# Kernel optimization log

Hardware: AMD Instinct MI355X
Metric: run time of the kernel (lower is better)

Reference implementation:

```python
import jax, jax.numpy as jnp
import numpy as np

B, N, IN_DIM, OUT = 4, 4096, 3, 40
NPTS = [1024, 256, 64, 16]   # base_points // sampling_ratio
K, FIRST_K = 8, 16
EPS = 1e-5

def gelu(t):
    return jax.nn.gelu(t, approximate=False)  # torch nn.GELU default (erf)

def pdist2(a, b):
    # a: (b,d,m), b: (b,d,n) -> squared pairwise distances (b,m,n)
    aa = jnp.sum(a * a, axis=1)[:, :, None]
    bb = jnp.sum(b * b, axis=1)[:, None, :]
    return aa + bb - 2.0 * jnp.einsum('bdm,bdn->bmn', a, b)

def knn_idx(a, b, k):
    # indices of k nearest points of b for each point of a
    return jax.lax.top_k(-pdist2(a, b), k)[1]

def gather_nbr(x, ind):
    # x: (b,d,n), ind: (b,m,k) -> (b,d,m,k)
    b, d, n = x.shape
    m, k = ind.shape[1], ind.shape[2]
    idx = jnp.broadcast_to(ind.reshape(b, 1, m * k), (b, d, m * k))
    return jnp.take_along_axis(x, idx, axis=2).reshape(b, d, m, k)

def bn(x):
    # BatchNorm (training-mode batch stats, gamma=1, beta=0 as at init)
    ax = (0,) + tuple(range(2, x.ndim))
    mu = jnp.mean(x, axis=ax, keepdims=True)
    var = jnp.mean((x - mu) ** 2, axis=ax, keepdims=True)
    return (x - mu) / jnp.sqrt(var + EPS)

def route(x, nbr):
    # (b,d,n),(b,n,k) -> (b,2d,n,k) : cat([neighbor - center, center])
    sel = gather_nbr(x, nbr)
    xc = x[:, :, :, None]
    return jnp.concatenate([sel - xc, jnp.broadcast_to(xc, sel.shape)], axis=1)

def edge_conv(x, l1, l2, sc, k, nbr=None):
    if nbr is None:
        nbr = knn_idx(x, x, k)  # dynamic graph in feature space
    h = jnp.max(jnp.einsum('of,bfnk->bonk', l1, route(x, nbr)), axis=-1)
    h = gelu(bn(h))
    h = jnp.max(jnp.einsum('of,bfnk->bonk', l2, route(h, nbr)), axis=-1)
    short = x if sc is None else jnp.einsum('of,bfn->bon', sc, x)
    return gelu(bn(short + h))

def fps(xyz, m):
    # farthest point sampling; xyz: (b,3,n) -> indices (b,m); start index 0
    pts = jnp.transpose(xyz, (0, 2, 1))  # (b,n,3)
    b, n, _ = pts.shape
    def body(carry, _):
        dmin, last = carry
        lp = jnp.take_along_axis(pts, last[:, None, None], axis=1)  # (b,1,3)
        d = jnp.sum((pts - lp) ** 2, axis=-1)
        dmin = jnp.minimum(dmin, d)
        nxt = jnp.argmax(dmin, axis=-1).astype(jnp.int32)
        return (dmin, nxt), last
    init = (jnp.full((b, n), jnp.inf, pts.dtype), jnp.zeros((b,), jnp.int32))
    _, inds = jax.lax.scan(body, init, None, length=m)
    return jnp.transpose(inds)  # (b,m)

def _forward(x, xyz, mlp_w, mlp_b, c0_l1, c0_l2, l1s, l2s, scs,
             head_w1, head_w2, head_b2):
    b = x.shape[0]
    nbr0 = knn_idx(xyz, xyz, FIRST_K)
    h = gelu(bn(jnp.einsum('oi,bin->bon', mlp_w, x) + mlp_b[None, :, None]))
    h = edge_conv(h, c0_l1, c0_l2, None, FIRST_K, nbr=nbr0)
    cur = xyz
    for i in range(4):
        m = NPTS[i]
        sind = fps(cur, m)
        sxyz = jnp.take_along_axis(
            cur, jnp.broadcast_to(sind[:, None, :], (b, cur.shape[1], m)), axis=2)
        nbr = knn_idx(sxyz, cur, K)
        cur = jnp.mean(gather_nbr(cur, nbr), axis=-1)      # sampled xyz = nbr mean
        h = jnp.max(gather_nbr(h, nbr), axis=-1)           # sampled feat = nbr max
        h = edge_conv(h, l1s[i], l2s[i], scs[i], K)
    g = jnp.mean(h, axis=-1)                               # global average pool
    g = gelu(bn(g @ head_w1.T))
    return g @ head_w2.T + head_b2[None, :]


def setup_inputs() -> dict:
    key = jax.random.key(0)
    ks = jax.random.split(key, 20)
    def w(k, o, i):
        return (jax.random.normal(k, (o, i), jnp.float32) / np.sqrt(i)).astype(jnp.float32)
    return {
        'x': jax.random.normal(ks[0], (B, IN_DIM, N), jnp.float32),
        'xyz': jax.random.normal(ks[1], (B, 3, N), jnp.float32),
        'mlp_w': w(ks[2], 64, IN_DIM), 'mlp_b': jnp.zeros((64,), jnp.float32),
        'c0_l1': w(ks[3], 64, 128), 'c0_l2': w(ks[4], 64, 128),
        's0_l1': w(ks[5], 64, 128), 's0_l2': w(ks[6], 64, 128),
        's1_l1': w(ks[7], 128, 128), 's1_l2': w(ks[8], 128, 256), 's1_sc': w(ks[9], 128, 64),
        's2_l1': w(ks[10], 256, 256), 's2_l2': w(ks[11], 256, 512), 's2_sc': w(ks[12], 256, 128),
        's3_l1': w(ks[13], 512, 512), 's3_l2': w(ks[14], 512, 1024), 's3_sc': w(ks[15], 512, 256),
        'head_w1': w(ks[16], 256, 512), 'head_w2': w(ks[17], OUT, 256),
        'head_b2': jnp.zeros((OUT,), jnp.float32),
    }


def reference(x, xyz, mlp_w, mlp_b, c0_l1, c0_l2, s0_l1, s0_l2,
              s1_l1, s1_l2, s1_sc, s2_l1, s2_l2, s2_sc, s3_l1, s3_l2, s3_sc,
              head_w1, head_w2, head_b2):
    return _forward(x, xyz, mlp_w, mlp_b, c0_l1, c0_l2,
                    (s0_l1, s1_l1, s2_l1, s3_l1),
                    (s0_l2, s1_l2, s2_l2, s3_l2),
                    (None, s1_sc, s2_sc, s3_sc),
                    head_w1, head_w2, head_b2)
```

## Files before the change

### kernel.cpp

```cpp
#include <hip/hip_runtime.h>
#include <math.h>

#define NCHUNK 32
typedef unsigned long long ull;

__device__ __forceinline__ float gelu_f(float v){
  return 0.5f*v*(1.0f+erff(v*0.70710678118654752440f));
}

__device__ __forceinline__ unsigned flipf(float d){
  unsigned u = __float_as_uint(d);
  return (u & 0x80000000u) ? ~u : (u | 0x80000000u);
}

__device__ __forceinline__ ull umin64(ull a, ull b){ return a < b ? a : b; }
__device__ __forceinline__ ull umax64(ull a, ull b){ return a > b ? a : b; }

template<int CTRL>
__device__ __forceinline__ ull dpp64(ull k){
  int lo = __builtin_amdgcn_update_dpp(0, (int)(unsigned)k,       CTRL, 0xF, 0xF, true);
  int hi = __builtin_amdgcn_update_dpp(0, (int)(unsigned)(k>>32), CTRL, 0xF, 0xF, true);
  return ((ull)(unsigned)hi<<32) | (unsigned)lo;
}
__device__ __forceinline__ ull rl64(ull k, int l){
  unsigned lo = (unsigned)__builtin_amdgcn_readlane((int)(unsigned)k, l);
  unsigned hi = (unsigned)__builtin_amdgcn_readlane((int)(unsigned)(k>>32), l);
  return ((ull)hi<<32) | lo;
}
__device__ __forceinline__ ull fmax64(ull a, ull b){
  return (ull)__double_as_longlong(fmax(__longlong_as_double((long long)a),
                                        __longlong_as_double((long long)b)));
}
__device__ __forceinline__ ull wave_fmax(ull k){
  k = fmax64(k, dpp64<0xB1>(k));
  k = fmax64(k, dpp64<0x4E>(k));
  k = fmax64(k, dpp64<0x141>(k));
  k = fmax64(k, dpp64<0x140>(k));
  ull a=rl64(k,0), b=rl64(k,16), c=rl64(k,32), d=rl64(k,48);
  return fmax64(fmax64(a,b), fmax64(c,d));
}
template<int CTRL>
__device__ __forceinline__ ull kmin_dpp(ull k){
  ull o = dpp64<CTRL>(k);
  return o < k ? o : k;
}
__device__ __forceinline__ ull wave_kmin(ull k){
  k = kmin_dpp<0xB1>(k);
  k = kmin_dpp<0x4E>(k);
  k = kmin_dpp<0x141>(k);
  k = kmin_dpp<0x140>(k);
  ull a=rl64(k,0), b=rl64(k,16), c=rl64(k,32), d=rl64(k,48);
  ull ab = a < b ? a : b, cd = c < d ? c : d;
  return ab < cd ? ab : cd;
}


template<int K, int T>
__device__ __forceinline__ void knn_body(
    const float* __restrict__ cand, int n,
    const float* __restrict__ qsrc, const int* __restrict__ qidx, int m,
    int* __restrict__ nbr, float* __restrict__ outc,
    int b, int qblk, int qoff, char* smem)
{
  float4* tile = (float4*)smem;
  constexpr int NWV = T/64;
  int wv = threadIdx.x >> 6, lane = threadIdx.x & 63;
  int q = qblk*NWV + wv + qoff;
  const float* cb = cand + (size_t)b*3*n;
  int qi = qidx ? qidx[(size_t)b*m + q] : q;
  const float* qb = qsrc + (size_t)b*3*n;
  float qx = qb[qi], qy = qb[n+qi], qz = qb[2*n+qi];
  float aa = (qx*qx + qy*qy) + qz*qz;

  ull a[K];
  #pragma unroll
  for (int k=0;k<K;k++) a[k] = ~0ull;

  for (int base=0; base<n; base+=1024){
    int cnt = min(1024, n-base);
    for (int j=threadIdx.x; j<cnt; j+=T){
      float x=cb[base+j], y=cb[n+base+j], z=cb[2*n+base+j];
      tile[j] = make_float4(x,y,z,(x*x+y*y)+z*z);
    }
    __syncthreads();
    int steps = cnt >> 6;
    for (int i=0;i<steps;i++){
      int j = lane + (i<<6);
      float4 c = tile[j];
      float d = aa + c.w - 2.0f*((qx*c.x+qy*c.y)+qz*c.z);
      ull key = ((ull)flipf(d)<<32) | (unsigned)(base+j);
      if (key < a[K-1]){
        #pragma unroll
        for (int k=K-1;k>=1;k--)
          a[k] = umin64(umax64(a[k-1], key), a[k]);
        a[0] = umin64(a[0], key);
      }
    }
    __syncthreads();
  }

  ull head = a[0];
  int res[K];
  #pragma unroll
  for (int r=0; r<K; r++){
    ull mk = wave_kmin(head);
    res[r] = (int)(unsigned)mk;
    if (head == mk){
      #pragma unroll
      for (int i2=0;i2<K-1;i2++) a[i2]=a[i2+1];
      a[K-1] = ~0ull;
      head = a[0];
    }
  }
  if (lane == 0){
    int* o = nbr + ((size_t)b*m + q)*K;
    #pragma unroll
    for (int r=0;r<K;r++) o[r] = res[r];
  }
  if (outc != nullptr && lane < 3){
    const float* cd = cb + (size_t)lane*n;
    float s=0;
    #pragma unroll
    for (int k=0;k<K;k++) s += cd[res[k]];
    outc[((size_t)b*3 + lane)*m + q] = s * (1.0f/K);
  }
}

template<int NP, int T, int M>
__device__ __forceinline__ void fps_mw_seg(const float* __restrict__ cur, int n,
                                           int* __restrict__ sind, float* __restrict__ gdmin,
                                           int b, int M0, int M1, char* smem)
{
  constexpr int NW = T/64;
  int tid = threadIdx.x;
  int wv = tid>>6;
  const float* cb = cur + (size_t)b*3*n;
  float4* lp = (float4*)smem;
  ull* wred = (ull*)(smem + sizeof(float4)*NP*T);
  float* gd = gdmin + (size_t)b*n;
  float px[NP], py[NP], pz[NP], dmin[NP];
  unsigned nj[NP];
  #pragma unroll
  for (int s=0;s<NP;s++){
    int j = tid + s*T;
    px[s]=cb[j]; py[s]=cb[n+j]; pz[s]=cb[2*n+j];
    dmin[s] = (M0==0) ? 1e30f : gd[j];
    nj[s] = (unsigned)(~j);
    lp[j] = make_float4(px[s],py[s],pz[s],0.f);
  }
  __syncthreads();
  int ci = (M0==0) ? 0 : sind[(size_t)b*M + (M0-1)];
  float4 w0 = lp[ci];
  float X = w0.x, Y = w0.y, Z = w0.z;
  if (M0==0 && tid==0) sind[(size_t)b*M] = 0;
  __builtin_amdgcn_s_setprio(3);
  int p = 0;
  int s0 = (M0==0) ? 1 : M0;
  for (int step=s0; step<M1; step++){
    ull key[NP];
    #pragma unroll
    for (int s=0;s<NP;s++){
      float dx=px[s]-X, dy=py[s]-Y, dz=pz[s]-Z;
      float d = (dx*dx + dy*dy) + dz*dz;
      float nd = fminf(dmin[s], d);
      dmin[s] = nd;
      key[s] = ((ull)__float_as_uint(nd)<<32) | nj[s];
    }
    #pragma unroll
    for (int w=NP; w>1; w>>=1)
      #pragma unroll
      for (int i=0;i<NP;i++) if (i < (w>>1))
        key[i] = fmax64(key[i], key[i+(w>>1)]);
    ull wk = wave_fmax(key[0]);
    if ((tid&63)==0) wred[p*NW + wv] = wk;
    __syncthreads();
    const ulonglong2* wp2 = (const ulonglong2*)(wred + p*NW);
    ulonglong2 m0 = wp2[0], m1 = wp2[1], m2 = wp2[2], m3 = wp2[3];
    ull gk = fmax64(fmax64(fmax64(m0.x,m0.y), fmax64(m1.x,m1.y)),
                    fmax64(fmax64(m2.x,m2.y), fmax64(m3.x,m3.y)));
    int gi = (int)(~(unsigned)gk);
    if (tid==0) sind[(size_t)b*M + step] = gi;
    float4 wp = lp[gi];
    X=wp.x; Y=wp.y; Z=wp.z;
    p ^= 1;
  }
  __builtin_amdgcn_s_setprio(0);
  #pragma unroll
  for (int s=0;s<NP;s++) gd[tid + s*T] = dmin[s];
}

template<int NP, int M>
__device__ __forceinline__ void fps_sw_body(const float* __restrict__ cur, int n,
                                            int* __restrict__ sind, int b, char* smem)
{
  int lane = threadIdx.x;
  const float* cb = cur + (size_t)b*3*n;
  float4* lp = (float4*)smem;
  float px[NP], py[NP], pz[NP], dmin[NP];
  unsigned nj[NP];
  #pragma unroll
  for (int s=0;s<NP;s++){
    int j = lane + s*64;
    px[s]=cb[j]; py[s]=cb[n+j]; pz[s]=cb[2*n+j]; dmin[s]=1e30f;
    nj[s] = (unsigned)(~j);
    lp[j] = make_float4(px[s],py[s],pz[s],0.f);
  }
  float X = lp[0].x, Y = lp[0].y, Z = lp[0].z;
  if (lane==0) sind[(size_t)b*M] = 0;
  __builtin_amdgcn_s_setprio(3);
  for (int step=1; step<M; step++){
    ull key[NP];
    #pragma unroll
    for (int s=0;s<NP;s++){
      float dx=px[s]-X, dy=py[s]-Y, dz=pz[s]-Z;
      float d = (dx*dx + dy*dy) + dz*dz;
      float nd = fminf(dmin[s], d);
      dmin[s] = nd;
      key[s] = ((ull)__float_as_uint(nd)<<32) | nj[s];
    }
    #pragma unroll
    for (int w=NP; w>1; w>>=1)
      #pragma unroll
      for (int i=0;i<NP;i++) if (i < (w>>1))
        key[i] = fmax64(key[i], key[i+(w>>1)]);
    ull gk = wave_fmax(key[0]);
    int gi = (int)(~(unsigned)gk);
    if (lane==0) sind[(size_t)b*M + step] = gi;
    float4 wp = lp[gi];
    X=wp.x; Y=wp.y; Z=wp.z;
  }
  __builtin_amdgcn_s_setprio(0);
}

template<bool DUAL, bool BN>
__device__ __forceinline__ void gemm_body(
    const float* __restrict__ A, const float* __restrict__ B,
    float* __restrict__ out0, float* __restrict__ out1,
    int M, int N, int Kd, int lda, int ldb, int ldo, int boff,
    long sA, long sB, long sO, const float* __restrict__ part, float invR,
    int bxi, int byi, int bzi, char* smem)
{
  A += (size_t)bzi * sA; B += (size_t)bzi * sB;
  float* o0 = out0 + (size_t)bzi * sO;
  float* o1 = DUAL ? (out1 + (size_t)bzi * sO) : nullptr;
  int rowBase = byi*64, colBase = bxi*64;
  float (*As)[64]  = (float(*)[64])smem;
  float (*Bs0)[64] = (float(*)[64])(smem + 4096);
  float (*Bs1)[64] = (float(*)[64])(smem + 8192);
  float* mu_s = (float*)(smem + 12288);
  float* var_s = mu_s + 512;
  int tid = threadIdx.x;
  if (BN){
    for (int oo=tid; oo<Kd; oo+=blockDim.x){
      float s=0, q=0;
      #pragma unroll 4
      for (int c=0;c<NCHUNK;c++){
        s += part[(size_t)c*1024 + oo];
        q += part[(size_t)(NCHUNK+c)*1024 + oo];
      }
      float mu = s*invR;
      mu_s[oo] = mu;
      var_s[oo] = q*invR - mu*mu;
    }
    __syncthreads();
  }
  int ty = tid>>4, tx = tid&15;
  float acc0[4][4] = {}, acc1[4][4] = {};
  int lr = tid>>2, lk = (tid&3)*4;
  for (int k0=0; k0<Kd; k0+=16) {
    float4 va = make_float4(0,0,0,0);
    int r = rowBase + lr;
    if (r < M) va = *(const float4*)(A + (size_t)r*lda + k0 + lk);
    if (BN){
      int c = k0 + lk;
      va.x = gelu_f((va.x - mu_s[c+0]) / sqrtf(var_s[c+0] + 1e-5f));
      va.y = gelu_f((va.y - mu_s[c+1]) / sqrtf(var_s[c+1] + 1e-5f));
      va.z = gelu_f((va.z - mu_s[c+2]) / sqrtf(var_s[c+2] + 1e-5f));
      va.w = gelu_f((va.w - mu_s[c+3]) / sqrtf(var_s[c+3] + 1e-5f));
    }
    As[lk+0][lr]=va.x; As[lk+1][lr]=va.y; As[lk+2][lr]=va.z; As[lk+3][lr]=va.w;
    float4 vb = make_float4(0,0,0,0), vb2 = make_float4(0,0,0,0);
    int c2 = colBase + lr;
    if (c2 < N) {
      vb = *(const float4*)(B + (size_t)c2*ldb + k0 + lk);
      if (DUAL) vb2 = *(const float4*)(B + (size_t)c2*ldb + boff + k0 + lk);
    }
    Bs0[lk+0][lr]=vb.x; Bs0[lk+1][lr]=vb.y; Bs0[lk+2][lr]=vb.z; Bs0[lk+3][lr]=vb.w;
    if (DUAL) {
      Bs1[lk+0][lr]=vb2.x-vb.x; Bs1[lk+1][lr]=vb2.y-vb.y;
      Bs1[lk+2][lr]=vb2.z-vb.z; Bs1[lk+3][lr]=vb2.w-vb.w;
    }
    __syncthreads();
    #pragma unroll
    for (int kk=0;kk<16;kk++){
      float4 a  = *(const float4*)&As[kk][ty*4];
      float4 b0 = *(const float4*)&Bs0[kk][tx*4];
      float av[4]={a.x,a.y,a.z,a.w};
      float b0v[4]={b0.x,b0.y,b0.z,b0.w};
      #pragma unroll
      for (int i=0;i<4;i++)
        #pragma unroll
        for (int j=0;j<4;j++) acc0[i][j] = fmaf(av[i], b0v[j], acc0[i][j]);
      if (DUAL) {
        float4 b1 = *(const float4*)&Bs1[kk][tx*4];
        float b1v[4]={b1.x,b1.y,b1.z,b1.w};
        #pragma unroll
        for (int i=0;i<4;i++)
          #pragma unroll
          for (int j=0;j<4;j++) acc1[i][j] = fmaf(av[i], b1v[j], acc1[i][j]);
      }
    }
    __syncthreads();
  }
  #pragma unroll
  for (int i=0;i<4;i++){
    int r = rowBase + ty*4 + i;
    if (r < M) {
      #pragma unroll
      for (int j=0;j<4;j++){
        int c = colBase + tx*4 + j;
        if (c < N) {
          o0[(size_t)r*ldo + c] = acc0[i][j];
          if (DUAL) o1[(size_t)r*ldo + c] = acc1[i][j];
        }
      }
    }
  }
}

template<bool DUAL, bool BN>
__device__ __forceinline__ void gemm_body_g(
    const float* __restrict__ A, const float* __restrict__ B,
    float* __restrict__ out0, float* __restrict__ out1,
    int M, int N, int Kd, int lda, int ldb, int ldo, int boff,
    const float* __restrict__ part, float invR,
    int bxi, int byi, char* smem)
{
  int rowBase = byi*64, colBase = bxi*64;
  float (*As)[64]  = (float(*)[64])smem;
  float (*Bs0)[64] = (float(*)[64])(smem + 4096);
  float (*Bs1)[64] = (float(*)[64])(smem + 8192);
  float* mu_s = (float*)(smem + 12288);
  float* var_s = mu_s + 512;
  int tid = threadIdx.x;
  bool act = tid < 256;
  if (BN){
    for (int oo=tid; oo<Kd; oo+=blockDim.x){
      float s=0, q=0;
      #pragma unroll 4
      for (int c=0;c<NCHUNK;c++){
        s += part[(size_t)c*1024 + oo];
        q += part[(size_t)(NCHUNK+c)*1024 + oo];
      }
      float mu = s*invR;
      mu_s[oo] = mu;
      var_s[oo] = q*invR - mu*mu;
    }
    __syncthreads();
  }
  int ty = tid>>4, tx = tid&15;
  float acc0[4][4] = {}, acc1[4][4] = {};
  int lr = tid>>2, lk = (tid&3)*4;
  for (int k0=0; k0<Kd; k0+=16) {
    if (act){
      float4 va = make_float4(0,0,0,0);
      int r = rowBase + lr;
      if (r < M) va = *(const float4*)(A + (size_t)r*lda + k0 + lk);
      if (BN){
        int c = k0 + lk;
        va.x = gelu_f((va.x - mu_s[c+0]) / sqrtf(var_s[c+0] + 1e-5f));
        va.y = gelu_f((va.y - mu_s[c+1]) / sqrtf(var_s[c+1] + 1e-5f));
        va.z = gelu_f((va.z - mu_s[c+2]) / sqrtf(var_s[c+2] + 1e-5f));
        va.w = gelu_f((va.w - mu_s[c+3]) / sqrtf(var_s[c+3] + 1e-5f));
      }
      As[lk+0][lr]=va.x; As[lk+1][lr]=va.y; As[lk+2][lr]=va.z; As[lk+3][lr]=va.w;
      float4 vb = make_float4(0,0,0,0), vb2 = make_float4(0,0,0,0);
      int c2 = colBase + lr;
      if (c2 < N) {
        vb = *(const float4*)(B + (size_t)c2*ldb + k0 + lk);
        if (DUAL) vb2 = *(const float4*)(B + (size_t)c2*ldb + boff + k0 + lk);
      }
      Bs0[lk+0][lr]=vb.x; Bs0[lk+1][lr]=vb.y; Bs0[lk+2][lr]=vb.z; Bs0[lk+3][lr]=vb.w;
      if (DUAL) {
        Bs1[lk+0][lr]=vb2.x-vb.x; Bs1[lk+1][lr]=vb2.y-vb.y;
        Bs1[lk+2][lr]=vb2.z-vb.z; Bs1[lk+3][lr]=vb2.w-vb.w;
      }
    }
    __syncthreads();
    if (act){
      #pragma unroll
      for (int kk=0;kk<16;kk++){
        float4 a  = *(const float4*)&As[kk][ty*4];
        float4 b0 = *(const float4*)&Bs0[kk][tx*4];
        float av[4]={a.x,a.y,a.z,a.w};
        float b0v[4]={b0.x,b0.y,b0.z,b0.w};
        #pragma unroll
        for (int i=0;i<4;i++)
          #pragma unroll
          for (int j=0;j<4;j++) acc0[i][j] = fmaf(av[i], b0v[j], acc0[i][j]);
        if (DUAL) {
          float4 b1 = *(const float4*)&Bs1[kk][tx*4];
          float b1v[4]={b1.x,b1.y,b1.z,b1.w};
          #pragma unroll
          for (int i=0;i<4;i++)
            #pragma unroll
            for (int j=0;j<4;j++) acc1[i][j] = fmaf(av[i], b1v[j], acc1[i][j]);
        }
      }
    }
    __syncthreads();
  }
  if (act){
    #pragma unroll
    for (int i=0;i<4;i++){
      int r = rowBase + ty*4 + i;
      if (r < M) {
        #pragma unroll
        for (int j=0;j<4;j++){
          int c = colBase + tx*4 + j;
          if (c < N) {
            out0[(size_t)r*ldo + c] = acc0[i][j];
            if (DUAL) out1[(size_t)r*ldo + c] = acc1[i][j];
          }
        }
      }
    }
  }
}

__device__ __forceinline__ void gather_elem(
    const float* __restrict__ P, const int* __restrict__ nbr,
    const float* __restrict__ addA, const float* __restrict__ addB,
    float* __restrict__ out, int n_out, int n_src, int O, int K, int total, int e)
{
  if (e >= total) return;
  int o = e % O; int r = e / O;
  int b = r / n_out; int i = r % n_out;
  const int* nb = nbr + ((size_t)b*n_out + i)*K;
  float mx = -1e38f;
  for (int k=0;k<K;k++){
    int j = nb[k];
    float v = P[((size_t)b*n_src + j)*O + o];
    mx = fmaxf(mx, v);
  }
  float res = mx;
  if (addA) res += addA[e];
  if (addB) res = addB[e] + res;
  out[e] = res;
}

__device__ __forceinline__ void gatherbn_body(
    const float* __restrict__ P, const int* __restrict__ nbr,
    const float* __restrict__ part, float invR,
    float* __restrict__ out, float* __restrict__ aa,
    int n_out, int n_src, int O, int K, int blk, char* smem)
{
  float* mu_s = (float*)smem; float* var_s = mu_s + 256; float* sv = var_s + 256;
  int tid = threadIdx.x;
  for (int oo=tid; oo<O; oo+=256){
    float s=0, q=0;
    #pragma unroll 4
    for (int c=0;c<NCHUNK;c++){
      s += part[(size_t)c*1024 + oo];
      q += part[(size_t)(NCHUNK+c)*1024 + oo];
    }
    float mu = s*invR;
    mu_s[oo] = mu;
    var_s[oo] = q*invR - mu*mu;
  }
  __syncthreads();
  int e = blk*256 + tid;
  int o = e % O; int r = e / O;
  int b = r / n_out; int i = r % n_out;
  const int* nb = nbr + ((size_t)b*n_out + i)*K;
  float mu = mu_s[o], sd = sqrtf(var_s[o] + 1e-5f);
  float mx = -1e38f;
  for (int k=0;k<K;k++){
    int j = nb[k];
    float p = P[((size_t)b*n_src + j)*O + o];
    float v = gelu_f((p - mu)/sd);
    mx = fmaxf(mx, v);
  }
  out[e] = mx;
  sv[tid] = mx*mx;
  __syncthreads();
  for (int st=O>>1; st>0; st>>=1){
    if (o < st) sv[tid] += sv[tid+st];
    __syncthreads();
  }
  if (o == 0) aa[r] = sv[tid];
}


#define FPS_SMEM 65664

__global__ __launch_bounds__(512,2) void mega1(
    const float* __restrict__ xyz, const float* __restrict__ x,
    const float* __restrict__ mlpw, const float* __restrict__ mlpb,
    int* __restrict__ sind0, float* __restrict__ gdmin,
    int* __restrict__ nbr0, float* __restrict__ hA, int M0, int M1)
{
  __shared__ __align__(16) char SMEM[FPS_SMEM];
  int bid = blockIdx.x;
  if (bid < 4){
    fps_mw_seg<8,512,1024>(xyz, 4096, sind0, gdmin, bid, M0, M1, SMEM);
  } else if (bid < 4+2048){
    int kb = bid - 4;
    knn_body<16,512>(xyz, 4096, xyz, nullptr, 4096, nbr0, nullptr, kb>>9, kb&511, 0, SMEM);
  } else {
    int e = (bid - 2052)*512 + threadIdx.x;
    if (e < 4*4096*64){
      int o = e & 63; int r = e >> 6;
      int b = r / 4096; int i = r % 4096;
      const float* xb = x + (size_t)b*3*4096;
      hA[e] = ((mlpw[o*3+0]*xb[i] + mlpw[o*3+1]*xb[4096+i]) + mlpw[o*3+2]*xb[2*4096+i]) + mlpb[o];
    }
  }
}

__global__ __launch_bounds__(512,2) void fps_bngelu(
    const float* fcur, int* sind, float* gdmin, int M0, int M1,
    float* __restrict__ xx, const float* __restrict__ part, float invR, int O, int total)
{
  __shared__ __align__(16) char SMEM[FPS_SMEM];
  if (blockIdx.x < 4){
    fps_mw_seg<8,512,1024>(fcur, 4096, sind, gdmin, blockIdx.x, M0, M1, SMEM);
    return;
  }
  float* mu_s = (float*)SMEM; float* var_s = mu_s + 512;
  for (int oo=threadIdx.x; oo<O; oo+=512){
    float s=0, q=0;
    #pragma unroll 4
    for (int c=0;c<NCHUNK;c++){
      s += part[(size_t)c*1024 + oo];
      q += part[(size_t)(NCHUNK+c)*1024 + oo];
    }
    float mu = s*invR;
    mu_s[oo] = mu;
    var_s[oo] = q*invR - mu*mu;
  }
  __syncthreads();
  int e = (blockIdx.x-4)*512 + threadIdx.x;
  if (e >= total) return;
  int o = e % O;
  float v = (xx[e]-mu_s[o]) / sqrtf(var_s[o] + 1e-5f);
  xx[e] = gelu_f(v);
}

template<bool DUAL, bool BN>
__global__ __launch_bounds__(512,2) void fps0_gemm(
    const float* fcur, int* sind, float* gdmin, int M0, int M1,
    const float* A, const float* B, float* out0, float* out1,
    int Mg, int Ng, int Kd, int lda, int ldb, int ldo, int boff,
    const float* part, float invR, int nbx)
{
  __shared__ __align__(16) char SMEM[FPS_SMEM];
  if (blockIdx.x < 4){
    fps_mw_seg<8,512,1024>(fcur, 4096, sind, gdmin, blockIdx.x, M0, M1, SMEM);
    return;
  }
  int l = blockIdx.x - 4;
  gemm_body_g<DUAL,BN>(A,B,out0,out1,Mg,Ng,Kd,lda,ldb,ldo,boff,part,invR, l%nbx, l/nbx, SMEM);
}

__global__ __launch_bounds__(512,2) void fps0_gather_knn(
    const float* fcur, int* sind, float* gdmin, int M0, int M1,
    const float* cand, int n, const float* qsrc, const int* qidx, int m,
    int* nbrOut, float* outc, int KNB,
    const float* P, const int* nbr, const float* addA, const float* addB,
    float* out, int n_out, int n_src, int O, int K, int total)
{
  __shared__ __align__(16) char SMEM[FPS_SMEM];
  if (blockIdx.x < 4){
    fps_mw_seg<8,512,1024>(fcur, 4096, sind, gdmin, blockIdx.x, M0, M1, SMEM);
    return;
  }
  int l = blockIdx.x - 4;
  if (l < KNB){
    knn_body<8,512>(cand, n, qsrc, qidx, m, nbrOut, outc, l>>6, l&63, 0, SMEM);
    return;
  }
  int e = (l-KNB)*512 + threadIdx.x;
  gather_elem(P, nbr, addA, addB, out, n_out, n_src, O, K, total, e);
}

__global__ __launch_bounds__(512,2) void fps0_gather(
    const float* fcur, int* sind, float* gdmin, int M0, int M1,
    const float* P, const int* nbr, const float* addA, const float* addB,
    float* out, int n_out, int n_src, int O, int K, int total)
{
  __shared__ __align__(16) char SMEM[FPS_SMEM];
  if (blockIdx.x < 4){
    fps_mw_seg<8,512,1024>(fcur, 4096, sind, gdmin, blockIdx.x, M0, M1, SMEM);
    return;
  }
  int e = (blockIdx.x-4)*512 + threadIdx.x;
  gather_elem(P, nbr, addA, addB, out, n_out, n_src, O, K, total, e);
}

__global__ __launch_bounds__(512,2) void fps0_stats(
    const float* fcur, int* sind, float* gdmin, int M0, int M1,
    const float* __restrict__ x, int R, int O, float* __restrict__ part)
{
  __shared__ __align__(16) char SMEM[FPS_SMEM];
  if (blockIdx.x < 4){
    fps_mw_seg<8,512,1024>(fcur, 4096, sind, gdmin, blockIdx.x, M0, M1, SMEM);
    return;
  }
  int o = threadIdx.x;
  if (o >= O) return;
  int chunk = blockIdx.x - 4;
  int per = (R + NCHUNK - 1)/NCHUNK;
  int r0 = chunk*per, r1 = min(r0+per, R);
  float s=0, q=0;
  for (int r=r0; r<r1; r++){ float v = x[(size_t)r*O + o]; s+=v; q+=v*v; }
  part[(size_t)chunk*1024 + o] = s;
  part[(size_t)(NCHUNK+chunk)*1024 + o] = q;
}

__global__ __launch_bounds__(256) void knn_wave8(
    const float* cand, int n, const float* qsrc, const int* qidx, int m, int qoff,
    int* nbr, float* outc)
{
  __shared__ __align__(16) char SMEM[16384];
  knn_body<8,256>(cand, n, qsrc, qidx, m, nbr, outc, blockIdx.y, blockIdx.x, qoff, SMEM);
}

template<int NP, int M>
__global__ __launch_bounds__(256) void fps_gatherbn(
    const float* fcur, int fn, int* sind,
    const float* P, const int* nbr, const float* part, float invR,
    float* out, float* aa, int n_out, int n_src, int O, int K)
{
  __shared__ __align__(16) char SMEM[(NP*64*16 > 16384) ? NP*64*16 : 16384];
  if (blockIdx.x < 4){
    if (threadIdx.x < 64) fps_sw_body<NP,M>(fcur, fn, sind, blockIdx.x, SMEM);
    return;
  }
  gatherbn_body(P, nbr, part, invR, out, aa, n_out, n_src, O, K, blockIdx.x-4, SMEM);
}

template<int NP, int M, bool DUAL, bool BN>
__global__ __launch_bounds__(256) void fps_gemm(
    const float* fcur, int fn, int* sind,
    const float* A, const float* B, float* out0, float* out1,
    int Mg, int Ng, int Kd, int lda, int ldb, int ldo, int boff,
    const float* part, float invR, int nbx, int nby)
{
  __shared__ __align__(16) char SMEM[(NP*64*16 > 16896) ? NP*64*16 : 16896];
  if (blockIdx.x < 4){
    if (threadIdx.x < 64) fps_sw_body<NP,M>(fcur, fn, sind, blockIdx.x, SMEM);
    return;
  }
  int l = blockIdx.x - 4;
  int bx = l % nbx, by = (l/nbx) % nby, bz = l/(nbx*nby);
  gemm_body<DUAL,BN>(A,B,out0,out1,Mg,Ng,Kd,lda,ldb,ldo,boff,0,0,0,part,invR,bx,by,bz,SMEM);
}

__global__ __launch_bounds__(256) void knn_gather(
    const float* cand, int n, const float* qsrc, const int* qidx, int m,
    int* nbrOut, float* outc, int KNB,
    const float* P, const int* nbr, const float* addA, const float* addB,
    float* out, int n_out, int n_src, int O, int K, int total)
{
  __shared__ __align__(16) char SMEM[16384];
  if (blockIdx.x < KNB){
    int qpb = m/4;
    knn_body<8,256>(cand, n, qsrc, qidx, m, nbrOut, outc, blockIdx.x/qpb, blockIdx.x%qpb, 0, SMEM);
    return;
  }
  gather_elem(P, nbr, addA, addB, out, n_out, n_src, O, K, total, (blockIdx.x-KNB)*256 + threadIdx.x);
}

__global__ __launch_bounds__(256) void knn_gemm(
    const float* cand, int n, const float* qsrc, const int* qidx, int m,
    int* nbrOut, float* outc, int KNB,
    const float* A, const float* B, float* out0,
    int Mg, int Ng, int Kd, int lda, int ldb, int ldo,
    long sA, long sB, long sO, int nbx, int nby)
{
  __shared__ __align__(16) char SMEM[16896];
  if (blockIdx.x < KNB){
    int qpb = m/4;
    knn_body<8,256>(cand, n, qsrc, qidx, m, nbrOut, outc, blockIdx.x/qpb, blockIdx.x%qpb, 0, SMEM);
    return;
  }
  int l = blockIdx.x - KNB;
  int bx = l % nbx, by = (l/nbx) % nby, bz = l/(nbx*nby);
  gemm_body<false,false>(A,B,out0,nullptr,Mg,Ng,Kd,lda,ldb,ldo,0,sA,sB,sO,nullptr,0.f,bx,by,bz,SMEM);
}

template<bool DUAL, bool BN>
__global__ __launch_bounds__(256) void gemm_nt(
    const float* A, const float* B, float* out0, float* out1,
    int M, int N, int Kd, int lda, int ldb, int ldo, int boff,
    long sA, long sB, long sO, const float* part, float invR)
{
  __shared__ __align__(16) char SMEM[16896];
  gemm_body<DUAL,BN>(A,B,out0,out1,M,N,Kd,lda,ldb,ldo,boff,sA,sB,sO,part,invR,
                     blockIdx.x, blockIdx.y, blockIdx.z, SMEM);
}

__global__ __launch_bounds__(256) void gemm2sc(
    const float* A2, const float* B2, float* o20, float* o21, int R, int O2, int O1v,
    const float* part, float invR,
    const float* Asc, const float* Bsc, float* osc, int Cin,
    int nbx, int nby)
{
  __shared__ __align__(16) char SMEM[16896];
  int l = blockIdx.x;
  int half = nbx*nby;
  if (l < half){
    gemm_body<true,true>(A2,B2,o20,o21,R,O2,O1v,O1v,2*O1v,O2,O1v,0,0,0,part,invR, l%nbx, l/nbx, 0, SMEM);
  } else {
    l -= half;
    gemm_body<false,false>(Asc,Bsc,osc,nullptr,R,O2,Cin,Cin,Cin,O2,0,0,0,0,nullptr,0.f, l%nbx, l/nbx, 0, SMEM);
  }
}

__global__ __launch_bounds__(256) void gathermax_kernel(
    const float* P, const int* nbr, const float* addA, const float* addB,
    float* out, int n_out, int n_src, int O, int K, int total)
{
  gather_elem(P, nbr, addA, addB, out, n_out, n_src, O, K, total, blockIdx.x*256 + threadIdx.x);
}

__global__ __launch_bounds__(256) void gatherbn_kernel(
    const float* P, const int* nbr, const float* part, float invR,
    float* out, float* aa, int n_out, int n_src, int O, int K)
{
  __shared__ __align__(16) char SMEM[3072];
  gatherbn_body(P, nbr, part, invR, out, aa, n_out, n_src, O, K, blockIdx.x, SMEM);
}

template<int K>
__global__ __launch_bounds__(256) void topk_wave(
    const float* __restrict__ G, const float* __restrict__ aa, int m,
    int* __restrict__ nbr)
{
  __shared__ float abs_s[1024];
  int b = blockIdx.y;
  int wv = threadIdx.x >> 6, lane = threadIdx.x & 63;
  int q = blockIdx.x*4 + wv;
  const float* ab = aa + (size_t)b*m;
  for (int j=threadIdx.x; j<m; j+=256) abs_s[j] = ab[j];
  __syncthreads();
  float aq = ab[q];
  const float* Gq = G + ((size_t)b*m + q)*m;

  ull a[K];
  #pragma unroll
  for (int k=0;k<K;k++) a[k] = ~0ull;

  int steps = (m+63)>>6;
  for (int i=0;i<steps;i++){
    int j = lane + (i<<6);
    ull key = ~0ull;
    if (j < m){
      float g = Gq[j];
      float d = aq + abs_s[j] - 2.0f*g;
      key = ((ull)flipf(d)<<32) | (unsigned)j;
    }
    if (key < a[K-1]){
      #pragma unroll
      for (int k=K-1;k>=1;k--)
        a[k] = umin64(umax64(a[k-1], key), a[k]);
      a[0] = umin64(a[0], key);
    }
  }
  ull head = a[0];
  int res[K];
  #pragma unroll
  for (int r=0; r<K; r++){
    ull mk = wave_kmin(head);
    res[r] = (int)(unsigned)mk;
    if (head == mk){
      #pragma unroll
      for (int i2=0;i2<K-1;i2++) a[i2]=a[i2+1];
      a[K-1] = ~0ull;
      head = a[0];
    }
  }
  if (lane == 0){
    int* o = nbr + ((size_t)b*m + q)*K;
    #pragma unroll
    for (int r=0;r<K;r++) o[r] = res[r];
  }
}

__global__ void stats_part_kernel(const float* __restrict__ x, int R, int O,
                                  float* __restrict__ part)
{
  int o = threadIdx.x;
  int chunk = blockIdx.x;
  int per = (R + NCHUNK - 1)/NCHUNK;
  int r0 = chunk*per, r1 = min(r0+per, R);
  float s=0, q=0;
  for (int r=r0; r<r1; r++){ float v = x[(size_t)r*O + o]; s+=v; q+=v*v; }
  part[(size_t)chunk*1024 + o] = s;
  part[(size_t)(NCHUNK+chunk)*1024 + o] = q;
}

__global__ __launch_bounds__(1024) void head_kernel(const float* __restrict__ h,
    const float* __restrict__ part, float invR,
    const float* __restrict__ w1, const float* __restrict__ w2,
    const float* __restrict__ b2, float* __restrict__ out)
{
  __shared__ __align__(16) float mu_s[512], var_s[512];
  __shared__ __align__(16) float g[4*512];
  __shared__ __align__(16) float t[4*256];
  int tid = threadIdx.x;
  for (int oo=tid; oo<512; oo+=1024){
    float s=0, q=0;
    #pragma unroll 4
    for (int c=0;c<NCHUNK;c++){
      s += part[(size_t)c*1024 + oo];
      q += part[(size_t)(NCHUNK+c)*1024 + oo];
    }
    float mu = s*invR;
    mu_s[oo] = mu;
    var_s[oo] = q*invR - mu*mu;
  }
  __syncthreads();
  for (int e=tid; e<2048; e+=1024){
    int b=e>>9, c=e&511;
    float mu = mu_s[c], sd = sqrtf(var_s[c] + 1e-5f);
    float s=0;
    for (int p=0;p<16;p++){
      float v = h[((size_t)(b*16+p))*512 + c];
      s += gelu_f((v-mu)/sd);
    }
    g[e] = s * (1.0f/16.0f);
  }
  __syncthreads();
  {
    int b = tid>>8, j = tid&255;
    const float4* gr = (const float4*)(g + b*512);
    const float4* wr = (const float4*)(w1 + (size_t)j*512);
    float s=0;
    for (int c=0;c<128;c++){
      float4 a=gr[c], w=wr[c];
      s = fmaf(a.x,w.x, fmaf(a.y,w.y, fmaf(a.z,w.z, fmaf(a.w,w.w, s))));
    }
    t[tid] = s;
  }
  __syncthreads();
  if (tid < 256){
    float v0=t[tid], v1=t[256+tid], v2=t[512+tid], v3=t[768+tid];
    float mu = ((v0+v1)+v2+v3)*0.25f;
    float d0=v0-mu, d1=v1-mu, d2=v2-mu, d3=v3-mu;
    float var = ((d0*d0+d1*d1)+d2*d2+d3*d3)*0.25f;
    float sq = sqrtf(var + 1e-5f);
    t[tid]     = gelu_f(d0/sq);
    t[256+tid] = gelu_f(d1/sq);
    t[512+tid] = gelu_f(d2/sq);
    t[768+tid] = gelu_f(d3/sq);
  }
  __syncthreads();
  if (tid < 160){
    int b = tid/40, o = tid%40;
    const float* tr = t + b*256; const float* wr = w2 + (size_t)o*256;
    float s=0;
    for (int j=0;j<256;j++) s = fmaf(tr[j], wr[j], s);
    out[tid] = s + b2[o];
  }
}

extern "C" void kernel_launch(void* const* d_in, const int* in_sizes, int n_in,
                              void* d_out, int out_size, void* d_ws, size_t ws_size,
                              hipStream_t stream)
{
  const float* x    = (const float*)d_in[0];
  const float* xyz  = (const float*)d_in[1];
  const float* mlpw = (const float*)d_in[2];
  const float* mlpb = (const float*)d_in[3];
  const float* c0l1 = (const float*)d_in[4];
  const float* c0l2 = (const float*)d_in[5];
  const float* L1[4] = {(const float*)d_in[6], (const float*)d_in[8],
                        (const float*)d_in[11], (const float*)d_in[14]};
  const float* L2[4] = {(const float*)d_in[7], (const float*)d_in[9],
                        (const float*)d_in[12], (const float*)d_in[15]};
  const float* SC[4] = {nullptr, (const float*)d_in[10],
                        (const float*)d_in[13], (const float*)d_in[16]};
  const float* hw1 = (const float*)d_in[17];
  const float* hw2 = (const float*)d_in[18];
  const float* hb2 = (const float*)d_in[19];
  float* out = (float*)d_out;

  float* ws = (float*)d_ws;
  const size_t MF = 1024*1024;
  float* D    = ws;
  float* hA   = ws + 4*MF;
  float* hX   = ws + 5*MF;
  float* hP   = ws + 6*MF;
  float* hCT  = ws + 7*MF;
  float* hSH  = ws + 8*MF;
  float* hH1  = ws + 9*MF;
  float* hOUT = ws + 10*MF;
  float* aux  = ws + 11*MF;
  int*   nbr0  = (int*)aux;                 aux += 262144;
  int*   nbrS0 = (int*)aux;                 aux += 32768;
  int*   nbrS1 = (int*)aux;                 aux += 8192;
  int*   nbrS2 = (int*)aux;                 aux += 2048;
  int*   nbrS3 = (int*)aux;                 aux += 512;
  int*   nbrF  = (int*)aux;                 aux += 32768;
  int*   sind0 = (int*)aux;                 aux += 4096;
  int*   sind1 = (int*)aux;                 aux += 1024;
  int*   sind2 = (int*)aux;                 aux += 256;
  int*   sind3 = (int*)aux;                 aux += 64;
  float* aa    = aux;                       aux += 4096;
  float* cur1  = aux;                       aux += 12288;
  float* cur2  = aux;                       aux += 3072;
  float* cur3  = aux;                       aux += 768;
  float* part  = aux;                       aux += 65536;
  float* gdmin = aux;                       aux += 16384;

  int tot0 = 4*4096*64;

  mega1<<<4100, 512, 0, stream>>>(xyz, x, mlpw, mlpb, sind0, gdmin, nbr0, hA, 0, 260);
  stats_part_kernel<<<NCHUNK, 64, 0, stream>>>(hA, 16384, 64, part);
  fps_bngelu<<<4+2048, 512, 0, stream>>>(xyz, sind0, gdmin, 260, 390, hA, part, 1.0f/16384.0f, 64, tot0);
  fps0_gemm<true,false><<<4+256, 512, 0, stream>>>(xyz, sind0, gdmin, 390, 517,
      hA, c0l1, hP, hCT, 16384, 64, 64, 64, 128, 64, 64, nullptr, 0.f, 1);
  fps0_gather_knn<<<4+256+2048, 512, 0, stream>>>(xyz, sind0, gdmin, 517, 644,
      xyz, 4096, xyz, sind0, 1024, nbrS0, cur1, 256,
      hP, nbr0, hCT, nullptr, hH1, 4096, 4096, 64, 16, 1048576);
  stats_part_kernel<<<NCHUNK, 64, 0, stream>>>(hH1, 16384, 64, part);
  fps0_gemm<true,true><<<4+256, 512, 0, stream>>>(xyz, sind0, gdmin, 644, 771,
      hH1, c0l2, hP, hCT, 16384, 64, 64, 64, 128, 64, 64, part, 1.0f/16384.0f, 1);
  fps0_gather<<<4+2048, 512, 0, stream>>>(xyz, sind0, gdmin, 771, 898,
      hP, nbr0, hCT, hA, hOUT, 4096, 4096, 64, 16, 1048576);
  fps0_stats<<<4+NCHUNK, 512, 0, stream>>>(xyz, sind0, gdmin, 898, 1024,
      hOUT, 16384, 64, part);

  knn_wave8<<<dim3(128,4),256,0,stream>>>(xyz, 4096, xyz, sind0, 1024, 512, nbrS0, cur1);

  fps_gatherbn<16,256><<<4+1024,256,0,stream>>>(cur1, 1024, sind1,
      hOUT, nbrS0, part, 1.0f/16384.0f, hX, aa, 1024, 4096, 64, 8);
  knn_gemm<<<256+1024,256,0,stream>>>(cur1, 1024, cur1, sind1, 256, nbrS1, cur2, 256,
      hX, hX, D, 1024, 1024, 64, 64, 64, 1024,
      (long)1024*64, (long)1024*64, (long)1024*1024, 16, 16);
  topk_wave<8><<<dim3(256,4),256,0,stream>>>(D, aa, 1024, nbrF);
  fps_gemm<4,64,true,false><<<4+64,256,0,stream>>>(cur2, 256, sind2,
      hX, L1[0], hP, hCT, 4096, 64, 64, 64, 128, 64, 64, nullptr, 0.f, 1, 64);
  knn_gather<<<64+1024,256,0,stream>>>(cur2, 256, cur2, sind2, 64, nbrS2, cur3, 64,
      hP, nbrF, hCT, nullptr, hH1, 1024, 1024, 64, 8, 262144);
  stats_part_kernel<<<NCHUNK, 64, 0, stream>>>(hH1, 4096, 64, part);
  fps_gemm<1,16,true,true><<<4+64,256,0,stream>>>(cur3, 64, sind3,
      hH1, L2[0], hP, hCT, 4096, 64, 64, 64, 128, 64, 64, part, 1.0f/4096.0f, 1, 64);
  knn_gather<<<16+1024,256,0,stream>>>(cur3, 64, cur3, sind3, 16, nbrS3, nullptr, 16,
      hP, nbrF, hCT, hX, hA, 1024, 1024, 64, 8, 262144);
  stats_part_kernel<<<NCHUNK, 64, 0, stream>>>(hA, 4096, 64, part);

  const int   mArr[3]   = {256, 64, 16};
  const int   nsrcArr[3]= {1024, 256, 64};
  const int   CinArr[3] = {64, 128, 256};
  const int   OArr[3]   = {128, 256, 512};
  const int*  nbrSs[3]  = {nbrS1, nbrS2, nbrS3};
  float* hcur = hA;
  float invRprev = 1.0f/4096.0f;
  for (int s=0;s<3;s++){
    int m = mArr[s], nsrc = nsrcArr[s], Cin = CinArr[s], O1 = OArr[s], O2 = OArr[s];
    int R = 4*m;
    int th = R*Cin;
    gatherbn_kernel<<<th/256,256,0,stream>>>(hcur, nbrSs[s], part, invRprev,
                                             hX, aa, m, nsrc, Cin, 8);
    dim3 gp((m+63)/64, (m+63)/64, 4);
    gemm_nt<false,false><<<gp,256,0,stream>>>(hX, hX, D, nullptr, m, m, Cin, Cin, Cin, m, 0,
                                              (long)m*Cin, (long)m*Cin, (long)m*m, nullptr, 0.f);
    topk_wave<8><<<dim3(m/4,4),256,0,stream>>>(D, aa, m, nbrF);
    dim3 gg1((O1+63)/64, (R+63)/64, 1);
    gemm_nt<true,false><<<gg1,256,0,stream>>>(hX, L1[s+1], hP, hCT, R, O1, Cin, Cin, 2*Cin, O1, Cin, 0,0,0, nullptr, 0.f);
    int t1 = R*O1;
    gathermax_kernel<<<(t1+255)/256,256,0,stream>>>(hP, nbrF, hCT, nullptr, hH1, m, m, O1, 8, t1);
    stats_part_kernel<<<NCHUNK, O1, 0, stream>>>(hH1, R, O1, part);
    int nbx = (O2+63)/64, nby = (R+63)/64;
    gemm2sc<<<2*nbx*nby,256,0,stream>>>(hH1, L2[s+1], hP, hCT, R, O2, O1, part, 1.0f/R,
                                        hX, SC[s+1], hSH, Cin, nbx, nby);
    int t2 = R*O2;
    float* outbuf = (s&1) ? hA : hOUT;
    gathermax_kernel<<<(t2+255)/256,256,0,stream>>>(hP, nbrF, hCT, hSH, outbuf, m, m, O2, 8, t2);
    stats_part_kernel<<<NCHUNK, O2, 0, stream>>>(outbuf, R, O2, part);
    hcur = outbuf;
    invRprev = 1.0f/R;
  }

  head_kernel<<<1,1024,0,stream>>>(hcur, part, 1.0f/64.0f, hw1, hw2, hb2, out);
}
```

Baseline: 1.690 ms.

## Split first-stage KNN across two waves per query and fuse Gram with layer-1 GEMM

The first-layer 16-NN search now splits each query's 4096 candidates across two wavefronts, each holding a sorted register list, and merges the two lists in shared memory. This doubles the knn block count inside the mega1 launch to give more parallelism per query. In the stage loop, the Gram-matrix GEMM and the dual layer-1 GEMM, which are independent, now run as one launch to remove a kernel launch and improve occupancy. The costs are an extra merge step and more blocks competing with the FPS blocks in mega1.

Measured after the change: 1.667 ms. Within noise of the previous version (-1.3%).

```diff
diff --git a/kernel.cpp b/kernel.cpp
--- a/kernel.cpp
+++ b/kernel.cpp
@@ -123,6 +123,74 @@
     #pragma unroll
     for (int k=0;k<K;k++) s += cd[res[k]];
     outc[((size_t)b*3 + lane)*m + q] = s * (1.0f/K);
+  }
+}
+
+__device__ __forceinline__ void knn16sp_body(
+    const float* __restrict__ cand, int n, int m,
+    int* __restrict__ nbr, int b, int qblk, char* smem)
+{
+  const int K = 16;
+  float4* tile = (float4*)smem;
+  ull* klist = (ull*)(smem + 16384);
+  int wv = threadIdx.x >> 6, lane = threadIdx.x & 63;
+  int qg = wv >> 1, half = wv & 1;
+  int q = qblk*4 + qg;
+  const float* cb = cand + (size_t)b*3*n;
+  float qx = cb[q], qy = cb[n+q], qz = cb[2*n+q];
+  float aa = (qx*qx + qy*qy) + qz*qz;
+
+  ull a[K];
+  #pragma unroll
+  for (int k=0;k<K;k++) a[k] = ~0ull;
+
+  for (int base=0; base<n; base+=1024){
+    for (int j=threadIdx.x; j<1024; j+=512){
+      float x=cb[base+j], y=cb[n+base+j], z=cb[2*n+base+j];
+      tile[j] = make_float4(x,y,z,(x*x+y*y)+z*z);
+    }
+    __syncthreads();
+    #pragma unroll
+    for (int i=0;i<8;i++){
+      int j = half*512 + lane + (i<<6);
+      float4 c = tile[j];
+      float d = aa + c.w - 2.0f*((qx*c.x+qy*c.y)+qz*c.z);
+      ull key = ((ull)flipf(d)<<32) | (unsigned)(base+j);
+      if (key < a[K-1]){
+        #pragma unroll
+        for (int k=K-1;k>=1;k--)
+          a[k] = umin64(umax64(a[k-1], key), a[k]);
+        a[0] = umin64(a[0], key);
+      }
+    }
+    __syncthreads();
+  }
+
+  ull head = a[0];
+  #pragma unroll
+  for (int r=0; r<K; r++){
+    ull mk = wave_kmin(head);
+    if (lane == 0) klist[(qg*2 + half)*K + r] = mk;
+    if (head == mk){
+      #pragma unroll
+      for (int i2=0;i2<K-1;i2++) a[i2]=a[i2+1];
+      a[K-1] = ~0ull;
+      head = a[0];
+    }
+  }
+  __syncthreads();
+  if (threadIdx.x < 4){
+    const ull* A = &klist[(threadIdx.x*2+0)*K];
+    const ull* B = &klist[(threadIdx.x*2+1)*K];
+    int ia=0, ib=0;
+    int* o = nbr + ((size_t)b*m + qblk*4 + threadIdx.x)*K;
+    #pragma unroll
+    for (int r=0;r<K;r++){
+      ull ka = A[ia], kb = B[ib];
+      bool ta = ka < kb;
+      o[r] = (int)(unsigned)(ta ? ka : kb);
+      ia += ta; ib += !ta;
+    }
   }
 }
 
@@ -504,11 +572,11 @@
   int bid = blockIdx.x;
   if (bid < 4){
     fps_mw_seg<8,512,1024>(xyz, 4096, sind0, gdmin, bid, M0, M1, SMEM);
-  } else if (bid < 4+2048){
+  } else if (bid < 4+4096){
     int kb = bid - 4;
-    knn_body<16,512>(xyz, 4096, xyz, nullptr, 4096, nbr0, nullptr, kb>>9, kb&511, 0, SMEM);
+    knn16sp_body(xyz, 4096, 4096, nbr0, kb>>10, kb&1023, SMEM);
   } else {
-    int e = (bid - 2052)*512 + threadIdx.x;
+    int e = (bid - 4100)*512 + threadIdx.x;
     if (e < 4*4096*64){
       int o = e & 63; int r = e >> 6;
       int b = r / 4096; int i = r % 4096;
@@ -688,6 +756,23 @@
   int l = blockIdx.x - KNB;
   int bx = l % nbx, by = (l/nbx) % nby, bz = l/(nbx*nby);
   gemm_body<false,false>(A,B,out0,nullptr,Mg,Ng,Kd,lda,ldb,ldo,0,sA,sB,sO,nullptr,0.f,bx,by,bz,SMEM);
+}
+
+__global__ __launch_bounds__(256) void gram_gemm(
+    const float* Ag, float* outg, int Mg, int Kg, long sAg, long sOg,
+    int ngx, int ngy, int NG,
+    const float* A2, const float* B2, float* o20, float* o21,
+    int M2, int N2, int K2, int boff2, int nb2x)
+{
+  __shared__ __align__(16) char SMEM[16896];
+  int l = blockIdx.x;
+  if (l < NG){
+    int bx = l % ngx, by = (l/ngx) % ngy, bz = l/(ngx*ngy);
+    gemm_body<false,false>(Ag,Ag,outg,nullptr,Mg,Mg,Kg,Kg,Kg,Mg,0,sAg,sAg,sOg,nullptr,0.f,bx,by,bz,SMEM);
+    return;
+  }
+  l -= NG;
+  gemm_body<true,false>(A2,B2,o20,o21,M2,N2,K2,K2,2*K2,N2,boff2,0,0,0,nullptr,0.f, l%nb2x, l/nb2x, 0, SMEM);
 }
 
 template<bool DUAL, bool BN>
@@ -917,7 +1002,7 @@
 
   int tot0 = 4*4096*64;
 
-  mega1<<<4100, 512, 0, stream>>>(xyz, x, mlpw, mlpb, sind0, gdmin, nbr0, hA, 0, 260);
+  mega1<<<6148, 512, 0, stream>>>(xyz, x, mlpw, mlpb, sind0, gdmin, nbr0, hA, 0, 260);
   stats_part_kernel<<<NCHUNK, 64, 0, stream>>>(hA, 16384, 64, part);
   fps_bngelu<<<4+2048, 512, 0, stream>>>(xyz, sind0, gdmin, 260, 390, hA, part, 1.0f/16384.0f, 64, tot0);
   fps0_gemm<true,false><<<4+256, 512, 0, stream>>>(xyz, sind0, gdmin, 390, 517,
@@ -965,12 +1050,13 @@
     int th = R*Cin;
     gatherbn_kernel<<<th/256,256,0,stream>>>(hcur, nbrSs[s], part, invRprev,
                                              hX, aa, m, nsrc, Cin, 8);
-    dim3 gp((m+63)/64, (m+63)/64, 4);
-    gemm_nt<false,false><<<gp,256,0,stream>>>(hX, hX, D, nullptr, m, m, Cin, Cin, Cin, m, 0,
-                                              (long)m*Cin, (long)m*Cin, (long)m*m, nullptr, 0.f);
+    int ngx = (m+63)/64, ngy = (m+63)/64;
+    int NG = ngx*ngy*4;
+    int nb1x = (O1+63)/64, nb1y = (R+63)/64;
+    gram_gemm<<<NG + nb1x*nb1y, 256, 0, stream>>>(
+        hX, D, m, Cin, (long)m*Cin, (long)m*m, ngx, ngy, NG,
+        hX, L1[s+1], hP, hCT, R, O1, Cin, Cin, nb1x);
     topk_wave<8><<<dim3(m/4,4),256,0,stream>>>(D, aa, m, nbrF);
-    dim3 gg1((O1+63)/64, (R+63)/64, 1);
-    gemm_nt<true,false><<<gg1,256,0,stream>>>(hX, L1[s+1], hP, hCT, R, O1, Cin, Cin, 2*Cin, O1, Cin, 0,0,0, nullptr, 0.f);
     int t1 = R*O1;
     gathermax_kernel<<<(t1+255)/256,256,0,stream>>>(hP, nbrF, hCT, nullptr, hH1, m, m, O1, 8, t1);
     stats_part_kernel<<<NCHUNK, O1, 0, stream>>>(hH1, R, O1, part);
```

## Use double-precision keys for top-k and fuse Gram and L1 GEMM launches

Applied to the files above, without the earlier changes.

The KNN insertion sort and wave-wide min reduction now pack distance and index into a double (flipped distance times 4096 plus index). This lets fmin/fmax replace 64-bit integer compare/select pairs. Separately, the per-stage Gram-matrix GEMM and the dual L1 projection GEMM are merged into one launch via block-index dispatch, removing a kernel launch per stage. The double encoding assumes indices below 4096 and exactly representable keys; it relies on FP64 throughput, and a flipped 32-bit value times 4096 stays within the 53-bit mantissa.

Result: faster. 1.558 ms (-7.8%).

```diff
diff --git a/kernel.cpp b/kernel.cpp
--- a/kernel.cpp
+++ b/kernel.cpp
@@ -12,9 +12,6 @@
   unsigned u = __float_as_uint(d);
   return (u & 0x80000000u) ? ~u : (u | 0x80000000u);
 }
-
-__device__ __forceinline__ ull umin64(ull a, ull b){ return a < b ? a : b; }
-__device__ __forceinline__ ull umax64(ull a, ull b){ return a > b ? a : b; }
 
 template<int CTRL>
 __device__ __forceinline__ ull dpp64(ull k){
@@ -40,18 +37,21 @@
   return fmax64(fmax64(a,b), fmax64(c,d));
 }
 template<int CTRL>
-__device__ __forceinline__ ull kmin_dpp(ull k){
-  ull o = dpp64<CTRL>(k);
-  return o < k ? o : k;
-}
-__device__ __forceinline__ ull wave_kmin(ull k){
-  k = kmin_dpp<0xB1>(k);
-  k = kmin_dpp<0x4E>(k);
-  k = kmin_dpp<0x141>(k);
-  k = kmin_dpp<0x140>(k);
-  ull a=rl64(k,0), b=rl64(k,16), c=rl64(k,32), d=rl64(k,48);
-  ull ab = a < b ? a : b, cd = c < d ? c : d;
-  return ab < cd ? ab : cd;
+__device__ __forceinline__ double dmin_dpp(double k){
+  ull o = dpp64<CTRL>((ull)__double_as_longlong(k));
+  return fmin(k, __longlong_as_double((long long)o));
+}
+__device__ __forceinline__ double wave_dmin(double k){
+  k = dmin_dpp<0xB1>(k);
+  k = dmin_dpp<0x4E>(k);
+  k = dmin_dpp<0x141>(k);
+  k = dmin_dpp<0x140>(k);
+  ull kb = (ull)__double_as_longlong(k);
+  double a = __longlong_as_double((long long)rl64(kb,0));
+  double b = __longlong_as_double((long long)rl64(kb,16));
+  double c = __longlong_as_double((long long)rl64(kb,32));
+  double d = __longlong_as_double((long long)rl64(kb,48));
+  return fmin(fmin(a,b), fmin(c,d));
 }
 
 
@@ -72,9 +72,9 @@
   float qx = qb[qi], qy = qb[n+qi], qz = qb[2*n+qi];
   float aa = (qx*qx + qy*qy) + qz*qz;
 
-  ull a[K];
+  double a[K];
   #pragma unroll
-  for (int k=0;k<K;k++) a[k] = ~0ull;
+  for (int k=0;k<K;k++) a[k] = 1e300;
 
   for (int base=0; base<n; base+=1024){
     int cnt = min(1024, n-base);
@@ -84,31 +84,33 @@
     }
     __syncthreads();
     int steps = cnt >> 6;
+    double jd = (double)(base + lane);
     for (int i=0;i<steps;i++){
       int j = lane + (i<<6);
       float4 c = tile[j];
       float d = aa + c.w - 2.0f*((qx*c.x+qy*c.y)+qz*c.z);
-      ull key = ((ull)flipf(d)<<32) | (unsigned)(base+j);
+      double key = (double)flipf(d) * 4096.0 + jd;
       if (key < a[K-1]){
         #pragma unroll
         for (int k=K-1;k>=1;k--)
-          a[k] = umin64(umax64(a[k-1], key), a[k]);
-        a[0] = umin64(a[0], key);
+          a[k] = fmin(fmax(a[k-1], key), a[k]);
+        a[0] = fmin(a[0], key);
       }
+      jd += 64.0;
     }
     __syncthreads();
   }
 
-  ull head = a[0];
+  double head = a[0];
   int res[K];
   #pragma unroll
   for (int r=0; r<K; r++){
-    ull mk = wave_kmin(head);
-    res[r] = (int)(unsigned)mk;
+    double mk = wave_dmin(head);
+    res[r] = (int)((ull)mk & 4095u);
     if (head == mk){
       #pragma unroll
       for (int i2=0;i2<K-1;i2++) a[i2]=a[i2+1];
-      a[K-1] = ~0ull;
+      a[K-1] = 1e300;
       head = a[0];
     }
   }
@@ -690,6 +692,23 @@
   gemm_body<false,false>(A,B,out0,nullptr,Mg,Ng,Kd,lda,ldb,ldo,0,sA,sB,sO,nullptr,0.f,bx,by,bz,SMEM);
 }
 
+__global__ __launch_bounds__(256) void gram_gemm(
+    const float* Ag, float* outg, int Mg, int Kg, long sAg, long sOg,
+    int ngx, int ngy, int NG,
+    const float* A2, const float* B2, float* o20, float* o21,
+    int M2, int N2, int K2, int boff2, int nb2x)
+{
+  __shared__ __align__(16) char SMEM[16896];
+  int l = blockIdx.x;
+  if (l < NG){
+    int bx = l % ngx, by = (l/ngx) % ngy, bz = l/(ngx*ngy);
+    gemm_body<false,false>(Ag,Ag,outg,nullptr,Mg,Mg,Kg,Kg,Kg,Mg,0,sAg,sAg,sOg,nullptr,0.f,bx,by,bz,SMEM);
+    return;
+  }
+  l -= NG;
+  gemm_body<true,false>(A2,B2,o20,o21,M2,N2,K2,K2,2*K2,N2,boff2,0,0,0,nullptr,0.f, l%nb2x, l/nb2x, 0, SMEM);
+}
+
 template<bool DUAL, bool BN>
 __global__ __launch_bounds__(256) void gemm_nt(
     const float* A, const float* B, float* out0, float* out1,
@@ -748,36 +767,38 @@
   float aq = ab[q];
   const float* Gq = G + ((size_t)b*m + q)*m;
 
-  ull a[K];
+  double a[K];
   #pragma unroll
-  for (int k=0;k<K;k++) a[k] = ~0ull;
+  for (int k=0;k<K;k++) a[k] = 1e300;
 
   int steps = (m+63)>>6;
+  double jd = (double)lane;
   for (int i=0;i<steps;i++){
     int j = lane + (i<<6);
-    ull key = ~0ull;
+    double key = 1e300;
     if (j < m){
       float g = Gq[j];
       float d = aq + abs_s[j] - 2.0f*g;
-      key = ((ull)flipf(d)<<32) | (unsigned)j;
+      key = (double)flipf(d) * 4096.0 + jd;
     }
     if (key < a[K-1]){
       #pragma unroll
       for (int k=K-1;k>=1;k--)
-        a[k] = umin64(umax64(a[k-1], key), a[k]);
-      a[0] = umin64(a[0], key);
-    }
-  }
-  ull head = a[0];
+        a[k] = fmin(fmax(a[k-1], key), a[k]);
+      a[0] = fmin(a[0], key);
+    }
+    jd += 64.0;
+  }
+  double head = a[0];
   int res[K];
   #pragma unroll
   for (int r=0; r<K; r++){
-    ull mk = wave_kmin(head);
-    res[r] = (int)(unsigned)mk;
+    double mk = wave_dmin(head);
+    res[r] = (int)((ull)mk & 4095u);
     if (head == mk){
       #pragma unroll
       for (int i2=0;i2<K-1;i2++) a[i2]=a[i2+1];
-      a[K-1] = ~0ull;
+      a[K-1] = 1e300;
       head = a[0];
     }
   }
@@ -965,12 +986,13 @@
     int th = R*Cin;
     gatherbn_kernel<<<th/256,256,0,stream>>>(hcur, nbrSs[s], part, invRprev,
                                              hX, aa, m, nsrc, Cin, 8);
-    dim3 gp((m+63)/64, (m+63)/64, 4);
-    gemm_nt<false,false><<<gp,256,0,stream>>>(hX, hX, D, nullptr, m, m, Cin, Cin, Cin, m, 0,
-                                              (long)m*Cin, (long)m*Cin, (long)m*m, nullptr, 0.f);
+    int ngx = (m+63)/64, ngy = (m+63)/64;
+    int NG = ngx*ngy*4;
+    int nb1x = (O1+63)/64, nb1y = (R+63)/64;
+    gram_gemm<<<NG + nb1x*nb1y, 256, 0, stream>>>(
+        hX, D, m, Cin, (long)m*Cin, (long)m*m, ngx, ngy, NG,
+        hX, L1[s+1], hP, hCT, R, O1, Cin, Cin, nb1x);
     topk_wave<8><<<dim3(m/4,4),256,0,stream>>>(D, aa, m, nbrF);
-    dim3 gg1((O1+63)/64, (R+63)/64, 1);
-    gemm_nt<true,false><<<gg1,256,0,stream>>>(hX, L1[s+1], hP, hCT, R, O1, Cin, Cin, 2*Cin, O1, Cin, 0,0,0, nullptr, 0.f);
     int t1 = R*O1;
     gathermax_kernel<<<(t1+255)/256,256,0,stream>>>(hP, nbrF, hCT, nullptr, hH1, m, m, O1, 8, t1);
     stats_part_kernel<<<NCHUNK, O1, 0, stream>>>(hH1, R, O1, part);
```
